# Optimization experiments

Hardware: AMD Instinct MI355X
Metric: run time of the kernel (lower is better)

## Reference

```python
import jax, jax.numpy as jnp
import numpy as np


def setup_inputs() -> dict:
    key = jax.random.key(0)
    k1, k2, k3 = jax.random.split(key, 3)
    B, T, D = 64, 256, 512
    real = jax.random.normal(k1, (B, T, D), dtype=jnp.float32)
    imag = jax.random.normal(k2, (B, T, D), dtype=jnp.float32)
    weight = jax.random.uniform(k3, (B, T, 1), dtype=jnp.float32)
    return {"real": real, "imag": imag, "weight": weight}


def reference(real, imag, weight):
    # Weighted complex outer-product mixture:
    #   out_r[b] = sum_t w[b,t] * (r_t r_t^T + i_t i_t^T)
    #   out_i[b] = sum_t w[b,t] * (i_t r_t^T - r_t i_t^T)
    # Equivalent to the original per-sample loop + TxDxD outer products,
    # but fused: scale one operand by w and contract over t directly.
    w = weight[..., 0]  # [B, T]
    rw = real * w[..., None]  # [B, T, D]
    iw = imag * w[..., None]
    out_r = jnp.einsum('btd,bte->bde', rw, real) + jnp.einsum('btd,bte->bde', iw, imag)
    out_i = jnp.einsum('btd,bte->bde', iw, real) - jnp.einsum('btd,bte->bde', rw, imag)
    return (out_r, out_i)
```

## Files before the change

kernel.cpp:

```cpp
#include <hip/hip_runtime.h>
#include <cstdint>
#include <cstddef>
#include <cmath>

#define BB 64
#define TT 256
#define DD 512
#define BK 32
#define TILEM 64
#define NITER (TT / BK)
#define NTILE 36
#define SUBSZ 4096
#define BUFSZ 16384

typedef short bf16x8 __attribute__((ext_vector_type(8)));
typedef float f32x4  __attribute__((ext_vector_type(4)));
typedef int   i32x4  __attribute__((ext_vector_type(4)));

static __device__ __forceinline__ unsigned short f2bf(float x) {
  unsigned u = __builtin_bit_cast(unsigned, x) + 0x8000u;
  return (unsigned short)(u >> 16);
}

__global__ __launch_bounds__(256, 3)
void ComplexMixture_54838142435828_kernel(const float* __restrict__ re,
                                          const float* __restrict__ im,
                                          const float* __restrict__ wt,
                                          float* __restrict__ out) {
  __shared__ __attribute__((aligned(16))) char smem[2 * BUFSZ];

  const int tid = threadIdx.x;

  const int L = blockIdx.x;
  const int c = L & 7;
  const int s = L >> 3;
  const int b  = c * 8 + s / NTILE;
  const int t  = s % NTILE;
  int ti = (int)((sqrtf(8.f * (float)t + 1.f) - 1.f) * 0.5f);
  if ((ti + 1) * (ti + 2) / 2 <= t) ++ti;
  if (ti * (ti + 1) / 2 > t) --ti;
  const int tj = t - ti * (ti + 1) / 2;
  const int d0 = ti * TILEM;
  const int e0 = tj * TILEM;

  const int lane = tid & 63;
  const int wid  = tid >> 6;
  const int wm   = (wid >> 1) * 32;
  const int wn   = (wid & 1) * 32;
  const int quad = lane >> 4;
  const int l16  = lane & 15;

  const bool aside = (wid < 2);
  const float* src = (wid & 1) ? im : re;
  const int panel  = aside ? d0 : e0;
  const int subOff = wid * SUBSZ;
  const int tq = lane & 15;
  const int th = lane >> 4;

  int wgo[4];
  #pragma unroll
  for (int dd = 0; dd < 4; ++dd)
    wgo[dd] = (th * 64 + 4 * tq + (dd ^ (tq & 3) ^ ((tq >> 2) & 1))) * 16;

  const size_t colBase = (size_t)(b * TT) * DD + panel + tq * 4;
  const float* wtb = wt + b * TT;

  f32x4 accR[2][2], accI[2][2];
  #pragma unroll
  for (int mt = 0; mt < 2; ++mt)
    #pragma unroll
    for (int nt = 0; nt < 2; ++nt) {
      accR[mt][nt] = (f32x4){0.f, 0.f, 0.f, 0.f};
      accI[mt][nt] = (f32x4){0.f, 0.f, 0.f, 0.f};
    }

  f32x4 v[8];
  f32x4 w0 = (f32x4){1.f,1.f,1.f,1.f}, w1 = w0;

  #pragma unroll
  for (int k = 0; k < 8; ++k)
    v[k] = *(const f32x4*)(src + colBase + (size_t)(th * 8 + k) * DD);
  if (aside) {
    w0 = *(const f32x4*)(wtb + th * 8);
    w1 = *(const f32x4*)(wtb + th * 8 + 4);
  }
  {
    char* wb = smem + subOff;
    if (aside) {
      #pragma unroll
      for (int k = 0; k < 4; ++k) v[k] *= w0[k];
      #pragma unroll
      for (int k = 0; k < 4; ++k) v[k + 4] *= w1[k];
    }
    #pragma unroll
    for (int dd = 0; dd < 4; ++dd) {
      union { unsigned short hh[8]; i32x4 q; } u;
      #pragma unroll
      for (int j = 0; j < 8; ++j) u.hh[j] = f2bf(v[j][dd]);
      *(i32x4*)(wb + wgo[dd]) = u.q;
    }
  }

  #pragma unroll
  for (int it = 0; it < NITER; ++it) {
    const int ktn = it * BK + BK;
    const int rbo = (it & 1) * BUFSZ;

    if (ktn < TT) {
      #pragma unroll
      for (int k = 0; k < 8; ++k)
        v[k] = *(const f32x4*)(src + colBase + (size_t)(ktn + th * 8 + k) * DD);
      if (aside) {
        w0 = *(const f32x4*)(wtb + ktn + th * 8);
        w1 = *(const f32x4*)(wtb + ktn + th * 8 + 4);
      }
    }

    asm volatile("s_waitcnt lgkmcnt(0)\n\ts_barrier" ::: "memory");

    const char* rb = smem + rbo;
    bf16x8 aR[2], aI[2], bR[2], bI[2];
    #pragma unroll
    for (int mt = 0; mt < 2; ++mt) {
      const int r  = wm + mt * 16 + l16;
      const int gi = (quad * 64 + (r & ~3) +
                      ((r & 3) ^ ((r >> 2) & 3) ^ ((r >> 4) & 1))) * 16;
      aR[mt] = *(const bf16x8*)(rb + gi);
      aI[mt] = *(const bf16x8*)(rb + SUBSZ + gi);
    }
    #pragma unroll
    for (int nt = 0; nt < 2; ++nt) {
      const int r  = wn + nt * 16 + l16;
      const int gi = (quad * 64 + (r & ~3) +
                      ((r & 3) ^ ((r >> 2) & 3) ^ ((r >> 4) & 1))) * 16;
      bR[nt] = *(const bf16x8*)(rb + 2 * SUBSZ + gi);
      bI[nt] = *(const bf16x8*)(rb + 3 * SUBSZ + gi);
    }

    #pragma unroll
    for (int mt = 0; mt < 2; ++mt) {
      const bf16x8 aRn = aR[mt] ^ (bf16x8)((short)0x8000);
      #pragma unroll
      for (int nt = 0; nt < 2; ++nt) {
        accR[mt][nt] = __builtin_amdgcn_mfma_f32_16x16x32_bf16(aR[mt], bR[nt], accR[mt][nt], 0, 0, 0);
        accR[mt][nt] = __builtin_amdgcn_mfma_f32_16x16x32_bf16(aI[mt], bI[nt], accR[mt][nt], 0, 0, 0);
        accI[mt][nt] = __builtin_amdgcn_mfma_f32_16x16x32_bf16(aI[mt], bR[nt], accI[mt][nt], 0, 0, 0);
        accI[mt][nt] = __builtin_amdgcn_mfma_f32_16x16x32_bf16(aRn,    bI[nt], accI[mt][nt], 0, 0, 0);
      }
    }

    if (ktn < TT) {
      char* wb = smem + ((it & 1) ^ 1) * BUFSZ + subOff;
      if (aside) {
        #pragma unroll
        for (int k = 0; k < 4; ++k) v[k] *= w0[k];
        #pragma unroll
        for (int k = 0; k < 4; ++k) v[k + 4] *= w1[k];
      }
      #pragma unroll
      for (int dd = 0; dd < 4; ++dd) {
        union { unsigned short hh[8]; i32x4 q; } u;
        #pragma unroll
        for (int j = 0; j < 8; ++j) u.hh[j] = f2bf(v[j][dd]);
        *(i32x4*)(wb + wgo[dd]) = u.q;
      }
    }
  }

  const size_t NOFF = (size_t)BB * DD * DD;
  float* tbR = (float*)(smem + wid * SUBSZ);
  float* tbI = tbR + 512;
  const bool offdiag = (ti != tj);

  #pragma unroll
  for (int mt = 0; mt < 2; ++mt) {
    #pragma unroll
    for (int nt = 0; nt < 2; ++nt)
      #pragma unroll
      for (int r = 0; r < 4; ++r) {
        const int a = (quad * 4 + r) * 32 + ((nt * 16 + l16) ^ (quad << 3));
        tbR[a] = accR[mt][nt][r];
        tbI[a] = accI[mt][nt][r];
      }
    {
      const int rowD = lane >> 2;
      const int ech  = (lane & 3) * 8;
      const int a0   = rowD * 32 + (ech ^ ((rowD >> 2) << 3));
      const f32x4 r0 = *(const f32x4*)&tbR[a0];
      const f32x4 r1 = *(const f32x4*)&tbR[a0 + 4];
      const f32x4 i0 = *(const f32x4*)&tbI[a0];
      const f32x4 i1 = *(const f32x4*)&tbI[a0 + 4];
      const size_t ro = ((size_t)(b * DD + d0 + wm + mt * 16 + rowD)) * DD
                      + (size_t)(e0 + wn + ech);
      *(f32x4*)&out[ro]            = r0;
      *(f32x4*)&out[ro + 4]        = r1;
      *(f32x4*)&out[NOFF + ro]     = i0;
      *(f32x4*)&out[NOFF + ro + 4] = i1;
    }
    if (offdiag) {
      const int er = lane & 31;
      const int hf = lane >> 5;
      f32x4 rr0, rr1, ii0, ii1;
      #pragma unroll
      for (int j2 = 0; j2 < 4; ++j2) {
        const int p0 = hf * 8 + j2;
        const int p1 = hf * 8 + 4 + j2;
        const int a0 = p0 * 32 + (er ^ ((p0 >> 2) << 3));
        const int a1 = p1 * 32 + (er ^ ((p1 >> 2) << 3));
        rr0[j2] =  tbR[a0];
        rr1[j2] =  tbR[a1];
        ii0[j2] = -tbI[a0];
        ii1[j2] = -tbI[a1];
      }
      const size_t mo = ((size_t)(b * DD + e0 + wn + er)) * DD
                      + (size_t)(d0 + wm + mt * 16 + hf * 8);
      *(f32x4*)&out[mo]            = rr0;
      *(f32x4*)&out[mo + 4]        = rr1;
      *(f32x4*)&out[NOFF + mo]     = ii0;
      *(f32x4*)&out[NOFF + mo + 4] = ii1;
    }
  }
}

extern "C" void kernel_launch(void* const* d_in, const int* in_sizes, int n_in,
                              void* d_out, int out_size, void* d_ws, size_t ws_size,
                              hipStream_t stream) {
  const float* re = (const float*)d_in[0];
  const float* im = (const float*)d_in[1];
  const float* wt = (const float*)d_in[2];
  float* out = (float*)d_out;
  ComplexMixture_54838142435828_kernel<<<dim3(BB * NTILE), dim3(256), 0, stream>>>(re, im, wt, out);
}
```

Baseline: 211.6 us.

## Precompute sqrt-weighted, transposed bf16 operands in a prep kernel before the GEMM

Adds a prep kernel that scales real and imag by sqrt(weight), converts them to bf16, and writes them transposed (D-major over T) into workspace. The main kernel then loads packed bf16 rows directly into LDS, with no per-iteration scaling or conversion. Each input is re-read by many tiles, so this halves the bytes those repeated loads pull in and drops the conversion ALU work. The cost is an extra launch plus a workspace round trip, and sqrt-weight scaling on both operands changes rounding (and assumes non-negative weights). The old fused kernel is kept as a fallback when no workspace is available.

```diff
diff --git a/kernel.cpp b/kernel.cpp
--- a/kernel.cpp
+++ b/kernel.cpp
@@ -22,10 +22,51 @@
   return (unsigned short)(u >> 16);
 }
 
-__global__ __launch_bounds__(256, 3)
-void ComplexMixture_54838142435828_kernel(const float* __restrict__ re,
-                                          const float* __restrict__ im,
-                                          const float* __restrict__ wt,
+__global__ __launch_bounds__(256, 4)
+void ComplexMixture_prep_kernel(const float* __restrict__ re,
+                                const float* __restrict__ im,
+                                const float* __restrict__ wt,
+                                unsigned short* __restrict__ ws) {
+  __shared__ float tile[64][65];
+  const int L  = blockIdx.x;
+  const int b  = L >> 5;
+  const int tt = (L >> 3) & 3;
+  const int dt = L & 7;
+  const int t0 = tt * 64, d0 = dt * 64;
+  const int tid = threadIdx.x;
+  const int rr = tid >> 4, rc = (tid & 15) * 4;
+  const int dr = tid >> 2, tc = (tid & 3) * 16;
+
+  #pragma unroll
+  for (int a = 0; a < 2; ++a) {
+    const float* in = a ? im : re;
+    unsigned short* ob = ws + (size_t)a * BB * DD * TT;
+    if (a) __syncthreads();
+    #pragma unroll
+    for (int p = 0; p < 4; ++p) {
+      const int trow = p * 16 + rr;
+      const float s = sqrtf(wt[b * TT + t0 + trow]);
+      const f32x4 v = *(const f32x4*)(in + ((size_t)(b * TT + t0 + trow)) * DD + d0 + rc);
+      tile[trow][rc + 0] = v[0] * s;
+      tile[trow][rc + 1] = v[1] * s;
+      tile[trow][rc + 2] = v[2] * s;
+      tile[trow][rc + 3] = v[3] * s;
+    }
+    __syncthreads();
+    union { unsigned short h[8]; i32x4 q; } u0, u1;
+    #pragma unroll
+    for (int j = 0; j < 8; ++j) {
+      u0.h[j] = f2bf(tile[tc + j][dr]);
+      u1.h[j] = f2bf(tile[tc + 8 + j][dr]);
+    }
+    unsigned short* o = ob + ((size_t)(b * DD + d0 + dr)) * TT + t0 + tc;
+    *(i32x4*)o       = u0.q;
+    *(i32x4*)(o + 8) = u1.q;
+  }
+}
+
+__global__ __launch_bounds__(256, 4)
+void ComplexMixture_54838142435828_kernel(const unsigned short* __restrict__ ws,
                                           float* __restrict__ out) {
   __shared__ __attribute__((aligned(16))) char smem[2 * BUFSZ];
 
@@ -50,20 +91,13 @@
   const int quad = lane >> 4;
   const int l16  = lane & 15;
 
-  const bool aside = (wid < 2);
-  const float* src = (wid & 1) ? im : re;
-  const int panel  = aside ? d0 : e0;
+  const unsigned short* wsr = ws;
+  const unsigned short* wsi = ws + (size_t)BB * DD * TT;
+  const unsigned short* src = (wid & 1) ? wsi : wsr;
+  const int panel  = (wid < 2) ? d0 : e0;
   const int subOff = wid * SUBSZ;
-  const int tq = lane & 15;
-  const int th = lane >> 4;
-
-  int wgo[4];
-  #pragma unroll
-  for (int dd = 0; dd < 4; ++dd)
-    wgo[dd] = (th * 64 + 4 * tq + (dd ^ (tq & 3) ^ ((tq >> 2) & 1))) * 16;
-
-  const size_t colBase = (size_t)(b * TT) * DD + panel + tq * 4;
-  const float* wtb = wt + b * TT;
+  const unsigned short* gsrc = src + ((size_t)(b * DD + panel + lane)) * TT;
+  const int slotC = (lane & ~3) | ((lane & 3) ^ ((lane >> 2) & 3) ^ ((lane >> 4) & 1));
 
   f32x4 accR[2][2], accI[2][2];
   #pragma unroll
@@ -74,31 +108,16 @@
       accI[mt][nt] = (f32x4){0.f, 0.f, 0.f, 0.f};
     }
 
-  f32x4 v[8];
-  f32x4 w0 = (f32x4){1.f,1.f,1.f,1.f}, w1 = w0;
-
-  #pragma unroll
-  for (int k = 0; k < 8; ++k)
-    v[k] = *(const f32x4*)(src + colBase + (size_t)(th * 8 + k) * DD);
-  if (aside) {
-    w0 = *(const f32x4*)(wtb + th * 8);
-    w1 = *(const f32x4*)(wtb + th * 8 + 4);
-  }
+  i32x4 v[4];
+
+  #pragma unroll
+  for (int oc = 0; oc < 4; ++oc)
+    v[oc] = *(const i32x4*)(gsrc + oc * 8);
   {
     char* wb = smem + subOff;
-    if (aside) {
-      #pragma unroll
-      for (int k = 0; k < 4; ++k) v[k] *= w0[k];
-      #pragma unroll
-      for (int k = 0; k < 4; ++k) v[k + 4] *= w1[k];
-    }
-    #pragma unroll
-    for (int dd = 0; dd < 4; ++dd) {
-      union { unsigned short hh[8]; i32x4 q; } u;
-      #pragma unroll
-      for (int j = 0; j < 8; ++j) u.hh[j] = f2bf(v[j][dd]);
-      *(i32x4*)(wb + wgo[dd]) = u.q;
-    }
+    #pragma unroll
+    for (int oc = 0; oc < 4; ++oc)
+      *(i32x4*)(wb + (oc * 64 + slotC) * 16) = v[oc];
   }
 
   #pragma unroll
@@ -108,12 +127,8 @@
 
     if (ktn < TT) {
       #pragma unroll
-      for (int k = 0; k < 8; ++k)
-        v[k] = *(const f32x4*)(src + colBase + (size_t)(ktn + th * 8 + k) * DD);
-      if (aside) {
-        w0 = *(const f32x4*)(wtb + ktn + th * 8);
-        w1 = *(const f32x4*)(wtb + ktn + th * 8 + 4);
-      }
+      for (int oc = 0; oc < 4; ++oc)
+        v[oc] = *(const i32x4*)(gsrc + ktn + oc * 8);
     }
 
     asm volatile("s_waitcnt lgkmcnt(0)\n\ts_barrier" ::: "memory");
@@ -151,19 +166,9 @@
 
     if (ktn < TT) {
       char* wb = smem + ((it & 1) ^ 1) * BUFSZ + subOff;
-      if (aside) {
-        #pragma unroll
-        for (int k = 0; k < 4; ++k) v[k] *= w0[k];
-        #pragma unroll
-        for (int k = 0; k < 4; ++k) v[k + 4] *= w1[k];
-      }
-      #pragma unroll
-      for (int dd = 0; dd < 4; ++dd) {
-        union { unsigned short hh[8]; i32x4 q; } u;
-        #pragma unroll
-        for (int j = 0; j < 8; ++j) u.hh[j] = f2bf(v[j][dd]);
-        *(i32x4*)(wb + wgo[dd]) = u.q;
-      }
+      #pragma unroll
+      for (int oc = 0; oc < 4; ++oc)
+        *(i32x4*)(wb + (oc * 64 + slotC) * 16) = v[oc];
     }
   }
 
@@ -222,6 +227,189 @@
   }
 }
 
+__global__ __launch_bounds__(256, 3)
+void ComplexMixture_fb_kernel(const float* __restrict__ re,
+                              const float* __restrict__ im,
+                              const float* __restrict__ wt,
+                              float* __restrict__ out) {
+  __shared__ __attribute__((aligned(16))) char smem[2 * BUFSZ];
+  const int tid = threadIdx.x;
+  const int L = blockIdx.x;
+  const int c = L & 7;
+  const int s = L >> 3;
+  const int b  = c * 8 + s / NTILE;
+  const int t  = s % NTILE;
+  int ti = (int)((sqrtf(8.f * (float)t + 1.f) - 1.f) * 0.5f);
+  if ((ti + 1) * (ti + 2) / 2 <= t) ++ti;
+  if (ti * (ti + 1) / 2 > t) --ti;
+  const int tj = t - ti * (ti + 1) / 2;
+  const int d0 = ti * TILEM;
+  const int e0 = tj * TILEM;
+  const int lane = tid & 63;
+  const int wid  = tid >> 6;
+  const int wm   = (wid >> 1) * 32;
+  const int wn   = (wid & 1) * 32;
+  const int quad = lane >> 4;
+  const int l16  = lane & 15;
+  const bool aside = (wid < 2);
+  const float* src = (wid & 1) ? im : re;
+  const int panel  = aside ? d0 : e0;
+  const int subOff = wid * SUBSZ;
+  const int tq = lane & 15;
+  const int th = lane >> 4;
+  int wgo[4];
+  #pragma unroll
+  for (int dd = 0; dd < 4; ++dd)
+    wgo[dd] = (th * 64 + 4 * tq + (dd ^ (tq & 3) ^ ((tq >> 2) & 1))) * 16;
+  const size_t colBase = (size_t)(b * TT) * DD + panel + tq * 4;
+  const float* wtb = wt + b * TT;
+  f32x4 accR[2][2], accI[2][2];
+  #pragma unroll
+  for (int mt = 0; mt < 2; ++mt)
+    #pragma unroll
+    for (int nt = 0; nt < 2; ++nt) {
+      accR[mt][nt] = (f32x4){0.f, 0.f, 0.f, 0.f};
+      accI[mt][nt] = (f32x4){0.f, 0.f, 0.f, 0.f};
+    }
+  f32x4 v[8];
+  f32x4 w0 = (f32x4){1.f,1.f,1.f,1.f}, w1 = w0;
+  #pragma unroll
+  for (int k = 0; k < 8; ++k)
+    v[k] = *(const f32x4*)(src + colBase + (size_t)(th * 8 + k) * DD);
+  if (aside) {
+    w0 = *(const f32x4*)(wtb + th * 8);
+    w1 = *(const f32x4*)(wtb + th * 8 + 4);
+  }
+  {
+    char* wb = smem + subOff;
+    if (aside) {
+      #pragma unroll
+      for (int k = 0; k < 4; ++k) v[k] *= w0[k];
+      #pragma unroll
+      for (int k = 0; k < 4; ++k) v[k + 4] *= w1[k];
+    }
+    #pragma unroll
+    for (int dd = 0; dd < 4; ++dd) {
+      union { unsigned short hh[8]; i32x4 q; } u;
+      #pragma unroll
+      for (int j = 0; j < 8; ++j) u.hh[j] = f2bf(v[j][dd]);
+      *(i32x4*)(wb + wgo[dd]) = u.q;
+    }
+  }
+  #pragma unroll
+  for (int it = 0; it < NITER; ++it) {
+    const int ktn = it * BK + BK;
+    const int rbo = (it & 1) * BUFSZ;
+    if (ktn < TT) {
+      #pragma unroll
+      for (int k = 0; k < 8; ++k)
+        v[k] = *(const f32x4*)(src + colBase + (size_t)(ktn + th * 8 + k) * DD);
+      if (aside) {
+        w0 = *(const f32x4*)(wtb + ktn + th * 8);
+        w1 = *(const f32x4*)(wtb + ktn + th * 8 + 4);
+      }
+    }
+    asm volatile("s_waitcnt lgkmcnt(0)\n\ts_barrier" ::: "memory");
+    const char* rb = smem + rbo;
+    bf16x8 aR[2], aI[2], bR[2], bI[2];
+    #pragma unroll
+    for (int mt = 0; mt < 2; ++mt) {
+      const int r  = wm + mt * 16 + l16;
+      const int gi = (quad * 64 + (r & ~3) +
+                      ((r & 3) ^ ((r >> 2) & 3) ^ ((r >> 4) & 1))) * 16;
+      aR[mt] = *(const bf16x8*)(rb + gi);
+      aI[mt] = *(const bf16x8*)(rb + SUBSZ + gi);
+    }
+    #pragma unroll
+    for (int nt = 0; nt < 2; ++nt) {
+      const int r  = wn + nt * 16 + l16;
+      const int gi = (quad * 64 + (r & ~3) +
+                      ((r & 3) ^ ((r >> 2) & 3) ^ ((r >> 4) & 1))) * 16;
+      bR[nt] = *(const bf16x8*)(rb + 2 * SUBSZ + gi);
+      bI[nt] = *(const bf16x8*)(rb + 3 * SUBSZ + gi);
+    }
+    #pragma unroll
+    for (int mt = 0; mt < 2; ++mt) {
+      const bf16x8 aRn = aR[mt] ^ (bf16x8)((short)0x8000);
+      #pragma unroll
+      for (int nt = 0; nt < 2; ++nt) {
+        accR[mt][nt] = __builtin_amdgcn_mfma_f32_16x16x32_bf16(aR[mt], bR[nt], accR[mt][nt], 0, 0, 0);
+        accR[mt][nt] = __builtin_amdgcn_mfma_f32_16x16x32_bf16(aI[mt], bI[nt], accR[mt][nt], 0, 0, 0);
+        accI[mt][nt] = __builtin_amdgcn_mfma_f32_16x16x32_bf16(aI[mt], bR[nt], accI[mt][nt], 0, 0, 0);
+        accI[mt][nt] = __builtin_amdgcn_mfma_f32_16x16x32_bf16(aRn,    bI[nt], accI[mt][nt], 0, 0, 0);
+      }
+    }
+    if (ktn < TT) {
+      char* wb = smem + ((it & 1) ^ 1) * BUFSZ + subOff;
+      if (aside) {
+        #pragma unroll
+        for (int k = 0; k < 4; ++k) v[k] *= w0[k];
+        #pragma unroll
+        for (int k = 0; k < 4; ++k) v[k + 4] *= w1[k];
+      }
+      #pragma unroll
+      for (int dd = 0; dd < 4; ++dd) {
+        union { unsigned short hh[8]; i32x4 q; } u;
+        #pragma unroll
+        for (int j = 0; j < 8; ++j) u.hh[j] = f2bf(v[j][dd]);
+        *(i32x4*)(wb + wgo[dd]) = u.q;
+      }
+    }
+  }
+  const size_t NOFF = (size_t)BB * DD * DD;
+  float* tbR = (float*)(smem + wid * SUBSZ);
+  float* tbI = tbR + 512;
+  const bool offdiag = (ti != tj);
+  #pragma unroll
+  for (int mt = 0; mt < 2; ++mt) {
+    #pragma unroll
+    for (int nt = 0; nt < 2; ++nt)
+      #pragma unroll
+      for (int r = 0; r < 4; ++r) {
+        const int a = (quad * 4 + r) * 32 + ((nt * 16 + l16) ^ (quad << 3));
+        tbR[a] = accR[mt][nt][r];
+        tbI[a] = accI[mt][nt][r];
+      }
+    {
+      const int rowD = lane >> 2;
+      const int ech  = (lane & 3) * 8;
+      const int a0   = rowD * 32 + (ech ^ ((rowD >> 2) << 3));
+      const f32x4 r0 = *(const f32x4*)&tbR[a0];
+      const f32x4 r1 = *(const f32x4*)&tbR[a0 + 4];
+      const f32x4 i0 = *(const f32x4*)&tbI[a0];
+      const f32x4 i1 = *(const f32x4*)&tbI[a0 + 4];
+      const size_t ro = ((size_t)(b * DD + d0 + wm + mt * 16 + rowD)) * DD
+                      + (size_t)(e0 + wn + ech);
+      *(f32x4*)&out[ro]            = r0;
+      *(f32x4*)&out[ro + 4]        = r1;
+      *(f32x4*)&out[NOFF + ro]     = i0;
+      *(f32x4*)&out[NOFF + ro + 4] = i1;
+    }
+    if (offdiag) {
+      const int er = lane & 31;
+      const int hf = lane >> 5;
+      f32x4 rr0, rr1, ii0, ii1;
+      #pragma unroll
+      for (int j2 = 0; j2 < 4; ++j2) {
+        const int p0 = hf * 8 + j2;
+        const int p1 = hf * 8 + 4 + j2;
+        const int a0 = p0 * 32 + (er ^ ((p0 >> 2) << 3));
+        const int a1 = p1 * 32 + (er ^ ((p1 >> 2) << 3));
+        rr0[j2] =  tbR[a0];
+        rr1[j2] =  tbR[a1];
+        ii0[j2] = -tbI[a0];
+        ii1[j2] = -tbI[a1];
+      }
+      const size_t mo = ((size_t)(b * DD + e0 + wn + er)) * DD
+                      + (size_t)(d0 + wm + mt * 16 + hf * 8);
+      *(f32x4*)&out[mo]            = rr0;
+      *(f32x4*)&out[mo + 4]        = rr1;
+      *(f32x4*)&out[NOFF + mo]     = ii0;
+      *(f32x4*)&out[NOFF + mo + 4] = ii1;
+    }
+  }
+}
+
 extern "C" void kernel_launch(void* const* d_in, const int* in_sizes, int n_in,
                               void* d_out, int out_size, void* d_ws, size_t ws_size,
                               hipStream_t stream) {
@@ -229,5 +417,12 @@
   const float* im = (const float*)d_in[1];
   const float* wt = (const float*)d_in[2];
   float* out = (float*)d_out;
-  ComplexMixture_54838142435828_kernel<<<dim3(BB * NTILE), dim3(256), 0, stream>>>(re, im, wt, out);
+  const size_t need = (size_t)2 * BB * DD * TT * sizeof(unsigned short);
+  if (d_ws != nullptr && ws_size >= need) {
+    unsigned short* ws = (unsigned short*)d_ws;
+    ComplexMixture_prep_kernel<<<dim3(BB * 32), dim3(256), 0, stream>>>(re, im, wt, ws);
+    ComplexMixture_54838142435828_kernel<<<dim3(BB * NTILE), dim3(256), 0, stream>>>(ws, out);
+  } else {
+    ComplexMixture_fb_kernel<<<dim3(BB * NTILE), dim3(256), 0, stream>>>(re, im, wt, out);
+  }
 }
```

New measurement: 234.1 us. 10.7% more time.
